# Kernel tuning notes

Hardware: AMD Instinct MI355X
Metric: run time of the kernel (lower is better)

The kernel has to match this reference:

```python
import jax, jax.numpy as jnp
import numpy as np

B, N, F, L = 16, 1536, 128, 2   # batch, input_features, enc(=dec)_features, n_layers
SLOPE = 0.2                      # LeakyReLU alpha
NEG = -1e9                       # mask fill for softmax


def setup_inputs() -> dict:
    key = jax.random.key(0)
    ks = jax.random.split(key, 14)
    g = lambda k, shape, s=0.05: (jax.random.normal(k, shape, jnp.float32) * s)
    data = jax.random.randint(ks[0], (B, N), 0, 2)          # binary presence vector
    embed = g(ks[1], (N + 1, F)).at[0].set(0.0)              # padding_idx=0 row zeroed
    return {
        "data": data,
        "embed": embed,
        "enc_W": g(ks[2], (L, F, F)),
        "enc_a_src": g(ks[3], (L, F)),
        "enc_a_dst": g(ks[4], (L, F)),
        "param_W": g(ks[5], (F, 2 * F)),
        "param_b": g(ks[6], (2 * F,)),
        "dec_W": g(ks[7], (F, F)),
        "dec_a_src": g(ks[8], (F,)),
        "dec_a_dst": g(ks[9], (F,)),
        "out_W1": g(ks[10], (F, F)),
        "out_b1": g(ks[11], (F,)),
        "out_W2": g(ks[12], (F, 1)),
        "out_b2": g(ks[13], (1,)),
    }


def _gat(x, mask, W, a_src, a_dst):
    """Single-head graph attention over a dense boolean adjacency `mask`.
    Equivalent to sparse GAT over the clique edge list data_to_edges() builds
    (self-loops included). Rows with no edges output 0."""
    h = x @ W                                    # (n, F)
    si = h @ a_src                               # (n,)
    sj = h @ a_dst                               # (n,)
    e = jax.nn.leaky_relu(si[:, None] + sj[None, :], SLOPE)
    e = jnp.where(mask, e, NEG)
    attn = jax.nn.softmax(e, axis=-1) * mask.any(axis=-1)[:, None]
    return attn @ h                              # (n, F)


def reference(data, embed, enc_W, enc_a_src, enc_a_dst, param_W, param_b,
              dec_W, dec_a_src, dec_a_dst, out_W1, out_b1, out_W2, out_b2):
    def per_sample(g):
        d = g != 0                               # active feature nodes
        m_in = d[:, None] & d[None, :]           # input clique adjacency (N, N)
        x = embed[:-1]                           # node features = embedding rows (N, F)
        for l in range(L):                       # encoder layers (n_layers=2)
            x = jax.nn.elu(_gat(x, m_in, enc_W[l], enc_a_src[l], enc_a_dst[l]))
        # variational parameterization (eval mode: dropout=id, reparam -> mean)
        par = x @ param_W + param_b              # (N, 2F)
        mean, sigma = par[:, :F], par[:, F:]
        w = (g == 1).astype(mean.dtype)
        cnt = jnp.maximum(w.sum(), 1.0)
        kld = 0.5 * jnp.sum(w[:, None] * (jnp.exp(sigma) - sigma - 1.0 + mean ** 2)) / cnt
        # append master node (last embedding row) and decode over extended clique
        enc_full = jnp.concatenate([mean, embed[-1:]], axis=0)      # (N+1, F)
        d_ext = jnp.concatenate([d, jnp.ones((1,), bool)])
        m_out = d_ext[:, None] & d_ext[None, :]                     # (N+1, N+1)
        dec = jax.nn.relu(_gat(enc_full, m_out, dec_W, dec_a_src, dec_a_dst))
        return dec[-1], kld                      # master-node readout (F,)

    feats, klds = jax.vmap(per_sample)(data)     # (B, F), (B,)
    pred = jax.nn.relu(feats @ out_W1 + out_b1) @ out_W2 + out_b2   # (B, 1)
    return pred, jnp.sum(klds)
```

## Files before the change

### kernel.cpp

```cpp
#include <hip/hip_runtime.h>

#define BB 16
#define NN 1536
#define FF 128
#define SLOPE 0.2f
#define NS 2048
#define CHS 64
#define NCH 24
#define TI 16
#define NPB (NN/8)
#define NDC 24

__global__ __launch_bounds__(1024) void k_sortpre(
    const int* __restrict__ data,
    const float* __restrict__ embed, const float* __restrict__ decW,
    const float* __restrict__ aS, const float* __restrict__ aD,
    const float* __restrict__ SJb, long sStride,
    int* __restrict__ actG, int* __restrict__ cntG,
    float* __restrict__ hN, float* __restrict__ sN,
    float* __restrict__ keyG, int* __restrict__ pjG,
    float* __restrict__ SBG, float* __restrict__ SDG)
{
  int b = blockIdx.x, t = threadIdx.x;
  if (b == BB){
    __shared__ float rs[2][2];
    if (t < FF){
      float acc = 0.f;
      for (int k=0;k<FF;++k) acc += embed[(long)NN*FF + k] * decW[k*FF + t];
      hN[t] = acc;
      float ps = acc * aS[t];
      float pd = acc * aD[t];
      #pragma unroll
      for (int o=32;o;o>>=1){ ps += __shfl_down(ps,o); pd += __shfl_down(pd,o); }
      if ((t&63)==0){ rs[0][t>>6]=ps; rs[1][t>>6]=pd; }
    }
    __syncthreads();
    if (t==0){ sN[0]=rs[0][0]+rs[0][1]; sN[1]=rs[1][0]+rs[1][1]; }
    return;
  }

  __shared__ float key[NS]; __shared__ int pj[NS];
  __shared__ float sb[NS]; __shared__ float sd[NS];
  __shared__ int cntS;
  int cnt;
  if (data != nullptr){
    __shared__ int s[256];
    const int PER = NN/256;
    int local[NN/256]; int nl = 0;
    if (t < 256){
      int base = t*PER;
      #pragma unroll
      for (int u=0; u<PER; ++u){
        if (data[b*NN + base + u] != 0) local[nl++] = base+u;
      }
      s[t]=nl;
    }
    __syncthreads();
    if (t==0){ int run=0; for (int i=0;i<256;i++){ int v=s[i]; s[i]=run; run+=v; }
               cntG[b]=run; cntS=run; }
    __syncthreads();
    if (t < 256){
      int o = s[t];
      for (int u=0; u<nl; ++u) actG[b*NN + o + u] = local[u];
    }
    __syncthreads();
    cnt = cntS;
  } else {
    cnt = cntG[b];
  }

  const float* SJ = SJb + (long)b*sStride;
  const int* act = (data != nullptr) ? actG + b*NN : nullptr;
  int NSort = 32; while (NSort < cnt) NSort <<= 1;

  for (int e=t; e<NSort; e+=1024){
    if (e<cnt){ int io = act ? act[e] : e; key[e]=SJ[io]; pj[e]=io; }
    else { key[e]=__builtin_inff(); pj[e]=0; }
  }
  __syncthreads();
  for (int k=2; k<=NSort; k<<=1){
    for (int j=k>>1; j>0; j>>=1){
      for (int e=t; e<NSort; e+=1024){
        int l = e ^ j;
        if (l > e){
          bool asc = ((e & k) == 0);
          float a0=key[e], a1=key[l];
          if (asc ? (a0>a1) : (a0<a1)){
            key[e]=a1; key[l]=a0; int p=pj[e]; pj[e]=pj[l]; pj[l]=p;
          }
        }
      }
      __syncthreads();
    }
  }
  for (int e=t; e<NSort; e+=1024){
    if (e<cnt){ float kk=key[e]; sb[e]=__expf(kk); sd[e]=__expf(SLOPE*kk); }
    else { sb[e]=0.f; sd[e]=0.f; }
  }
  __syncthreads();
  for (int off=1; off<NSort; off<<=1){
    float t0[2], t1[2]; int ne=0;
    for (int e=t; e<NSort; e+=1024){
      t0[ne] = (e>=off) ? sb[e-off] : 0.f;
      t1[ne] = (e>=off) ? sd[e-off] : 0.f;
      ne++;
    }
    __syncthreads();
    ne=0;
    for (int e=t; e<NSort; e+=1024){ sb[e]+=t0[ne]; sd[e]+=t1[ne]; ne++; }
    __syncthreads();
  }
  for (int e=t; e<cnt; e+=1024){
    keyG[(long)b*NN+e]=key[e]; pjG[(long)b*NN+e]=pj[e];
    SBG[(long)b*NN+e]=sb[e];   SDG[(long)b*NN+e]=sd[e];
  }
}

__global__ __launch_bounds__(128) void k_rowmm(const float* __restrict__ Xv,
    const float* __restrict__ W, const float* __restrict__ aS, const float* __restrict__ aD,
    float* __restrict__ H, float* __restrict__ SI, float* __restrict__ SJ)
{
  int r0 = blockIdx.x*8;
  int f = threadIdx.x;
  __shared__ float xs[8][FF];
  #pragma unroll
  for (int r=0;r<8;++r) xs[r][f] = Xv[(long)(r0+r)*FF + f];
  __syncthreads();
  float acc[8]={0.f,0.f,0.f,0.f,0.f,0.f,0.f,0.f};
  for (int k=0;k<FF;++k){
    float w = W[k*FF + f];
    #pragma unroll
    for (int r=0;r<8;++r) acc[r] += xs[r][k]*w;
  }
  float as = aS[f], ad = aD[f];
  __shared__ float red[2][8][2];
  #pragma unroll
  for (int r=0;r<8;++r){
    H[(long)(r0+r)*FF + f] = acc[r];
    float ps = acc[r]*as, pd = acc[r]*ad;
    #pragma unroll
    for (int o=32;o;o>>=1){ ps += __shfl_down(ps,o); pd += __shfl_down(pd,o); }
    if ((f&63)==0){ red[0][r][f>>6]=ps; red[1][r][f>>6]=pd; }
  }
  __syncthreads();
  if (f<8){
    SI[r0+f]=red[0][f][0]+red[0][f][1]; SJ[r0+f]=red[1][f][0]+red[1][f][1];
  }
}

__global__ __launch_bounds__(128) void k_chunk(
    const float* __restrict__ keyG, const int* __restrict__ pjG,
    const int* __restrict__ cntArr,
    const float* __restrict__ Hb, long hStride,
    float* __restrict__ PP, float* __restrict__ PM)
{
  int b = blockIdx.y, c = blockIdx.x, f = threadIdx.x;
  int cnt = cntArr[b];
  int k0 = c*CHS;
  if (k0 >= cnt) return;
  int k1 = k0+CHS; if (k1 > cnt) k1 = cnt;
  int kn = k1-k0;
  const float* H = Hb + (long)b*hStride + f;
  __shared__ int pjs[CHS]; __shared__ float wbs[CHS], wds[CHS];
  if (f < CHS && f < kn){
    float kk = keyG[(long)b*NN + k0 + f];
    pjs[f] = pjG[(long)b*NN + k0 + f];
    wbs[f] = __expf(kk);
    wds[f] = __expf(SLOPE*kk);
  }
  __syncthreads();
  float accB=0.f, accD=0.f;
  float hbuf[8];
  #pragma unroll
  for (int i=0;i<8;i++) hbuf[i] = (i<kn) ? H[(long)pjs[i]*FF] : 0.f;
  long obase = ((long)b*NN + k0)*FF + f;
  int k=0;
  for (; k+8<=kn; k+=8){
    #pragma unroll
    for (int u=0;u<8;u++){
      float hv = hbuf[u];
      int kp = k+u+8;
      hbuf[u] = (kp<kn) ? H[(long)pjs[kp]*FF] : 0.f;
      accB = fmaf(wbs[k+u], hv, accB);
      accD = fmaf(wds[k+u], hv, accD);
      PP[obase + (long)(k+u)*FF] = accB;
      PM[obase + (long)(k+u)*FF] = accD;
    }
  }
  for (; k<kn; ++k){
    float hv = H[(long)pjs[k]*FF];
    accB = fmaf(wbs[k], hv, accB);
    accD = fmaf(wds[k], hv, accD);
    PP[obase + (long)k*FF] = accB;
    PM[obase + (long)k*FF] = accD;
  }
}

__global__ __launch_bounds__(128) void k_aggout_mm(
    const float* __restrict__ keyG, const float* __restrict__ SBG, const float* __restrict__ SDG,
    const float* __restrict__ PP, const float* __restrict__ PM,
    const float* __restrict__ SI1, const int* __restrict__ actB,
    const int* __restrict__ cntArr,
    const float* __restrict__ W, const float* __restrict__ aS, const float* __restrict__ aD,
    float* __restrict__ Hout, float* __restrict__ SIo, float* __restrict__ SJo)
{
  int b = blockIdx.y;
  int cnt = cntArr[b];
  int r0 = blockIdx.x*TI;
  if (r0 >= cnt) return;
  int f = threadIdx.x;
  const int* act = actB + b*NN;
  __shared__ float keys[NN];
  __shared__ float offB[NCH][FF], offD[NCH][FF];
  __shared__ int kk[TI]; __shared__ float sis[TI];
  __shared__ float xs2[TI][FF];

  for (int e=f; e<cnt; e+=128) keys[e] = keyG[(long)b*NN + e];
  int nch = (cnt + CHS - 1)/CHS;
  for (int c=0; c<nch; ++c){
    int kend = (c+1)*CHS; if (kend > cnt) kend = cnt; kend -= 1;
    offB[c][f] = PP[((long)b*NN+kend)*FF+f];
    offD[c][f] = PM[((long)b*NN+kend)*FF+f];
  }
  float rb=0.f, rd=0.f;
  for (int c=0; c<nch; ++c){
    float tb=offB[c][f], td=offD[c][f];
    offB[c][f]=rb; offD[c][f]=rd;
    rb+=tb; rd+=td;
  }
  float TB = rb;
  __syncthreads();
  if (f < TI){
    int r = r0 + f;
    float si=0.f; int k=0;
    if (r < cnt){
      si = SI1[act[r]];
      float th = -si;
      int lo=0, hi=cnt;
      while (lo<hi){ int mid=(lo+hi)>>1; if (keys[mid]<=th) lo=mid+1; else hi=mid; }
      k = lo;
    }
    kk[f]=k; sis[f]=si;
  }
  __syncthreads();
  float TBs = SBG[(long)b*NN + (cnt-1)];
  int rmax = cnt - r0; if (rmax > TI) rmax = TI;
  for (int r=0; r<TI; ++r){
    float v = 0.f;
    if (r < rmax){
      int k = kk[r]; float si = sis[r];
      float PB=0.f, PD=0.f, SBv=0.f, SDv=0.f;
      if (k > 0){
        int c = (k-1)/CHS;
        PB = PP[((long)b*NN+(k-1))*FF+f] + offB[c][f];
        PD = PM[((long)b*NN+(k-1))*FF+f] + offD[c][f];
        SBv = SBG[(long)b*NN+(k-1)];
        SDv = SDG[(long)b*NN+(k-1)];
      }
      float ai=__expf(si), ci=__expf(SLOPE*si);
      float num = ai*(TB -PB ) + ci*PD;
      float den = ai*(TBs-SBv) + ci*SDv;
      float o2 = num/den;
      v = (o2>0.f)? o2 : (__expf(o2)-1.f);
    }
    xs2[r][f] = v;
  }
  __syncthreads();
  float acc2[TI];
  #pragma unroll
  for (int u=0;u<TI;++u) acc2[u]=0.f;
  for (int k=0;k<FF;++k){
    float w = W[k*FF + f];
    #pragma unroll
    for (int u=0;u<TI;++u) acc2[u] += xs2[u][k]*w;
  }
  float as = aS[f], ad = aD[f];
  __shared__ float red[2][TI][2];
  #pragma unroll
  for (int u=0;u<TI;++u){
    int rr=r0+u;
    if (rr<cnt) Hout[((long)b*NN+rr)*FF+f] = acc2[u];
    float ps = acc2[u]*as, pd = acc2[u]*ad;
    #pragma unroll
    for (int o=32;o;o>>=1){ ps += __shfl_down(ps,o); pd += __shfl_down(pd,o); }
    if ((f&63)==0){ red[0][u][f>>6]=ps; red[1][u][f>>6]=pd; }
  }
  __syncthreads();
  if (f < TI){
    int rr=r0+f;
    if (rr<cnt){
      SIo[(long)b*NN+rr]=red[0][f][0]+red[0][f][1];
      SJo[(long)b*NN+rr]=red[1][f][0]+red[1][f][1];
    }
  }
}

__global__ __launch_bounds__(128) void k_aggout(
    const float* __restrict__ keyG, const float* __restrict__ SBG, const float* __restrict__ SDG,
    const float* __restrict__ PP, const float* __restrict__ PM,
    const float* __restrict__ SIb,
    const int* __restrict__ cntArr, float* __restrict__ XoB)
{
  int b = blockIdx.y;
  int cnt = cntArr[b];
  int r0 = blockIdx.x*TI;
  if (r0 >= cnt) return;
  int f = threadIdx.x;
  const float* SI = SIb + (long)b*NN;
  float* xo = XoB + (long)b*NN*FF;
  __shared__ float keys[NN];
  __shared__ float offB[NCH][FF], offD[NCH][FF];
  __shared__ int kk[TI]; __shared__ float sis[TI];

  for (int e=f; e<cnt; e+=128) keys[e] = keyG[(long)b*NN + e];
  int nch = (cnt + CHS - 1)/CHS;
  for (int c=0; c<nch; ++c){
    int kend = (c+1)*CHS; if (kend > cnt) kend = cnt; kend -= 1;
    offB[c][f] = PP[((long)b*NN+kend)*FF+f];
    offD[c][f] = PM[((long)b*NN+kend)*FF+f];
  }
  float rb=0.f, rd=0.f;
  for (int c=0; c<nch; ++c){
    float tb=offB[c][f], td=offD[c][f];
    offB[c][f]=rb; offD[c][f]=rd;
    rb+=tb; rd+=td;
  }
  float TB = rb;
  __syncthreads();
  if (f < TI){
    int r = r0 + f;
    float si=0.f; int k=0;
    if (r < cnt){
      si = SI[r];
      float th = -si;
      int lo=0, hi=cnt;
      while (lo<hi){ int mid=(lo+hi)>>1; if (keys[mid]<=th) lo=mid+1; else hi=mid; }
      k = lo;
    }
    kk[f]=k; sis[f]=si;
  }
  __syncthreads();
  float TBs = SBG[(long)b*NN + (cnt-1)];
  int rmax = cnt - r0; if (rmax > TI) rmax = TI;
  for (int r=0; r<rmax; ++r){
    int k = kk[r]; float si = sis[r];
    float PB=0.f, PD=0.f, SBv=0.f, SDv=0.f;
    if (k > 0){
      int c = (k-1)/CHS;
      PB = PP[((long)b*NN+(k-1))*FF+f] + offB[c][f];
      PD = PM[((long)b*NN+(k-1))*FF+f] + offD[c][f];
      SBv = SBG[(long)b*NN+(k-1)];
      SDv = SDG[(long)b*NN+(k-1)];
    }
    float ai=__expf(si), ci=__expf(SLOPE*si);
    float num = ai*(TB -PB ) + ci*PD;
    float den = ai*(TBs-SBv) + ci*SDv;
    float o2 = num/den;
    xo[(long)(r0+r)*FF + f] = (o2>0.f)? o2 : (__expf(o2)-1.f);
  }
}

__global__ __launch_bounds__(256) void k_pardec(const float* __restrict__ XC,
    const float* __restrict__ pW, const float* __restrict__ pB,
    const float* __restrict__ decW, const float* __restrict__ dAd,
    float* __restrict__ KPART, float* __restrict__ H3, float* __restrict__ SJd,
    const int* __restrict__ cntArr)
{
  int b = blockIdx.y; int cnt = cntArr[b];
  int bx = blockIdx.x;
  int r0 = bx*8;
  int t = threadIdx.x;
  if (r0>=cnt){
    if (t==0) KPART[b*NPB + bx] = 0.f;
    return;
  }
  const float* X = XC + (long)b*NN*FF;
  __shared__ float xs[8][FF];
  for (int e=t; e<8*FF; e+=256){
    int r=e>>7, k=e&127; int rr=r0+r;
    xs[r][k] = (rr<cnt) ? X[(long)rr*FF+k] : 0.f;
  }
  __syncthreads();
  float acc[8]={0.f,0.f,0.f,0.f,0.f,0.f,0.f,0.f};
  for (int k=0;k<FF;++k){
    float w = pW[k*2*FF + t];
    #pragma unroll
    for (int r=0;r<8;++r) acc[r]+=xs[r][k]*w;
  }
  float bb = pB[t];
  float kacc=0.f;
  #pragma unroll
  for (int r=0;r<8;++r){
    int rr=r0+r;
    if (rr>=cnt) continue;
    float v = acc[r]+bb;
    if (t<FF) kacc += v*v;
    else kacc += __expf(v)-v-1.f;
  }
  #pragma unroll
  for (int o=32;o;o>>=1) kacc += __shfl_down(kacc,o);
  __shared__ float rw[4];
  if ((t&63)==0) rw[t>>6]=kacc;
  __syncthreads();
  if (t==0) KPART[b*NPB + bx] = rw[0]+rw[1]+rw[2]+rw[3];
  __shared__ float ms[8][FF];
  if (t < FF){
    #pragma unroll
    for (int r=0;r<8;++r){
      int rr=r0+r;
      ms[r][t] = (rr<cnt) ? acc[r]+bb : 0.f;
    }
  }
  __syncthreads();
  int h = t>>7, f = t&127;
  float a2[4]={0.f,0.f,0.f,0.f};
  for (int k=0;k<FF;++k){
    float w = decW[k*FF + f];
    #pragma unroll
    for (int u=0;u<4;++u) a2[u] += ms[h*4+u][k]*w;
  }
  float ad = dAd[f];
  __shared__ float redD[8][2];
  #pragma unroll
  for (int u=0;u<4;++u){
    int rq = h*4+u; int rr = r0+rq;
    if (rr<cnt) H3[((long)b*NN+rr)*FF+f] = a2[u];
    float pd = a2[u]*ad;
    #pragma unroll
    for (int o=32;o;o>>=1) pd += __shfl_down(pd,o);
    if ((t&63)==0) redD[rq][(t>>6)&1]=pd;
  }
  __syncthreads();
  if (t<8){
    int rr=r0+t;
    if (rr<cnt) SJd[(long)b*NN+rr]=redD[t][0]+redD[t][1];
  }
}

__global__ __launch_bounds__(128) void k_dec(const float* __restrict__ H3,
    const float* __restrict__ SJ3, const float* __restrict__ sN,
    const int* __restrict__ cntArr, float* __restrict__ DECP)
{
  int b=blockIdx.y, ch=blockIdx.x;
  int cnt=cntArr[b];
  int f=threadIdx.x;
  int r0=ch*CHS; int r1 = (r0+CHS < cnt) ? r0+CHS : cnt;
  float siN = sN[0];
  const float* H = H3 + (long)b*NN*FF;
  const float* SJ = SJ3 + (long)b*NN;
  float accV=0.f, accW=0.f;
  for (int r=r0;r<r1;++r){
    float sj=SJ[r]; float x=siN+sj;
    float e=(x>=0.f)? x : SLOPE*x;
    float w=__expf(e);
    accV += w*H[(long)r*FF+f];
    accW += w;
  }
  float* P = DECP + (long)(b*NDC+ch)*(FF+1);
  P[f]=accV;
  if (f==0) P[FF]=accW;
}

__global__ __launch_bounds__(128) void k_head(const float* __restrict__ DECP,
    const float* __restrict__ hN, const float* __restrict__ sN,
    const float* __restrict__ KPART, const int* __restrict__ cntArr,
    const float* __restrict__ W1, const float* __restrict__ b1,
    const float* __restrict__ W2, const float* __restrict__ b2,
    float* __restrict__ out)
{
  int b = blockIdx.x;
  int f = threadIdx.x;
  __shared__ float rw[2];
  if (b < BB){
    float siN=sN[0], sjN=sN[1];
    float xN=siN+sjN; float eN=(xN>=0.f)?xN:SLOPE*xN; float wN=__expf(eN);
    float num=0.f, den=0.f;
    for (int c=0;c<NDC;++c){
      const float* P = DECP + (long)(b*NDC+c)*(FF+1);
      num += P[f]; den += P[FF];
    }
    num += wN*hN[f]; den += wN;
    float v = num/den;
    __shared__ float feats[FF];
    feats[f] = (v>0.f)? v : 0.f;
    __syncthreads();
    float acc=0.f;
    for (int k=0;k<FF;++k) acc += feats[k]*W1[k*FF+f];
    acc += b1[f];
    acc = (acc>0.f)? acc : 0.f;
    float p = acc*W2[f];
    #pragma unroll
    for (int o=32;o;o>>=1) p += __shfl_down(p,o);
    if ((f&63)==0) rw[f>>6]=p;
    __syncthreads();
    if (f==0) out[b] = rw[0]+rw[1]+b2[0];
  } else {
    float s=0.f;
    for (int bb=0;bb<BB;++bb){
      float part=0.f;
      for (int c=f;c<NPB;c+=128) part += KPART[bb*NPB + c];
      #pragma unroll
      for (int o=32;o;o>>=1) part += __shfl_down(part,o);
      if ((f&63)==0) rw[f>>6]=part;
      __syncthreads();
      float tot = rw[0]+rw[1];
      int c=cntArr[bb]; float cf = (c>0)? (float)c : 1.f;
      s += 0.5f*tot/cf;
      __syncthreads();
    }
    if (f==0) out[16]=s;
  }
}

extern "C" void kernel_launch(void* const* d_in, const int* in_sizes, int n_in,
                              void* d_out, int out_size, void* d_ws, size_t ws_size,
                              hipStream_t stream)
{
  const int*   data  = (const int*)d_in[0];
  const float* embed = (const float*)d_in[1];
  const float* encW  = (const float*)d_in[2];
  const float* encAs = (const float*)d_in[3];
  const float* encAd = (const float*)d_in[4];
  const float* pW    = (const float*)d_in[5];
  const float* pB    = (const float*)d_in[6];
  const float* decW  = (const float*)d_in[7];
  const float* decAs = (const float*)d_in[8];
  const float* decAd = (const float*)d_in[9];
  const float* oW1   = (const float*)d_in[10];
  const float* oB1   = (const float*)d_in[11];
  const float* oW2   = (const float*)d_in[12];
  const float* oB2   = (const float*)d_in[13];
  float* out = (float*)d_out;

  float* w = (float*)d_ws;
  long o = 0;
  float* H1   = w+o; o += (long)NN*FF;
  float* H2   = w+o; o += (long)BB*NN*FF;
  float* XC   = w+o; o += (long)BB*NN*FF;
  float* PP   = w+o; o += (long)BB*NN*FF;
  float* PM   = w+o; o += (long)BB*NN*FF;
  float* SI1  = w+o; o += NN;
  float* SJ1  = w+o; o += NN;
  float* SI2  = w+o; o += (long)BB*NN;
  float* SJ2  = w+o; o += (long)BB*NN;
  float* KPART= w+o; o += (long)BB*NPB;
  float* hN   = w+o; o += FF;
  float* sN   = w+o; o += 2;
  float* DECP = w+o; o += (long)BB*NDC*(FF+1);
  float* keyG = w+o; o += (long)BB*NN;
  float* SBG  = w+o; o += (long)BB*NN;
  float* SDG  = w+o; o += (long)BB*NN;
  int* act = (int*)(w+o); o += (long)BB*NN;
  int* pjG = (int*)(w+o); o += (long)BB*NN;
  int* cnt = (int*)(w+o); o += BB;
  (void)in_sizes; (void)n_in; (void)out_size; (void)ws_size;

  k_rowmm<<<NN/8,128,0,stream>>>(embed, encW, encAs, encAd, H1, SI1, SJ1);
  k_sortpre<<<BB+1,1024,0,stream>>>(data, embed, decW, decAs, decAd,
      SJ1, 0L, act, cnt, hN, sN, keyG, pjG, SBG, SDG);
  k_chunk<<<dim3(NCH,BB),128,0,stream>>>(keyG, pjG, cnt, H1, 0L, PP, PM);
  k_aggout_mm<<<dim3(NN/TI,BB),128,0,stream>>>(keyG, SBG, SDG, PP, PM,
      SI1, act, cnt, encW + FF*FF, encAs + FF, encAd + FF, H2, SI2, SJ2);
  k_sortpre<<<BB,1024,0,stream>>>(nullptr, embed, decW, decAs, decAd,
      SJ2, (long)NN, act, cnt, hN, sN, keyG, pjG, SBG, SDG);
  k_chunk<<<dim3(NCH,BB),128,0,stream>>>(keyG, pjG, cnt, H2, (long)NN*FF, PP, PM);
  k_aggout<<<dim3(NN/TI,BB),128,0,stream>>>(keyG, SBG, SDG, PP, PM,
      SI2, cnt, XC);
  k_pardec<<<dim3(NPB,BB),256,0,stream>>>(XC, pW, pB, decW, decAd,
      KPART, H2 , SJ2 , cnt);
  k_dec<<<dim3(NDC,BB),128,0,stream>>>(H2 , SJ2, sN, cnt, DECP);
  k_head<<<BB+1,128,0,stream>>>(DECP, hN, sN, KPART, cnt, oW1, oB1, oW2, oB2, out);
}
```

Baseline: 276.1 us.

## Precompute chunk prefix offsets in separate kernel and shrink chunk and row tiles

Adds a k_offs kernel that computes the exclusive prefix sums of per-chunk totals once per batch. Previously every aggregation block recomputed these offsets into shared memory. Chunk size is halved to 32 so twice as many chunks run in parallel, and rows per aggregation block drop from 16 to 8, giving more blocks and less shared memory. The small matmul now reads four k values at a time from shared memory as float4. The cost is two extra kernel launches and global reads of the offset table.

```diff
diff --git a/kernel.cpp b/kernel.cpp
--- a/kernel.cpp
+++ b/kernel.cpp
@@ -5,10 +5,11 @@
 #define FF 128
 #define SLOPE 0.2f
 #define NS 2048
-#define CHS 64
-#define NCH 24
-#define TI 16
+#define CH2 32
+#define NCH2 48
+#define TI 8
 #define NPB (NN/8)
+#define DCS 64
 #define NDC 24
 
 __global__ __launch_bounds__(1024) void k_sortpre(
@@ -156,13 +157,13 @@
 {
   int b = blockIdx.y, c = blockIdx.x, f = threadIdx.x;
   int cnt = cntArr[b];
-  int k0 = c*CHS;
+  int k0 = c*CH2;
   if (k0 >= cnt) return;
-  int k1 = k0+CHS; if (k1 > cnt) k1 = cnt;
+  int k1 = k0+CH2; if (k1 > cnt) k1 = cnt;
   int kn = k1-k0;
   const float* H = Hb + (long)b*hStride + f;
-  __shared__ int pjs[CHS]; __shared__ float wbs[CHS], wds[CHS];
-  if (f < CHS && f < kn){
+  __shared__ int pjs[CH2]; __shared__ float wbs[CH2], wds[CH2];
+  if (f < CH2 && f < kn){
     float kk = keyG[(long)b*NN + k0 + f];
     pjs[f] = pjG[(long)b*NN + k0 + f];
     wbs[f] = __expf(kk);
@@ -196,9 +197,33 @@
   }
 }
 
+__global__ __launch_bounds__(128) void k_offs(
+    const float* __restrict__ PP, const float* __restrict__ PM,
+    const int* __restrict__ cntArr,
+    float* __restrict__ OFB, float* __restrict__ OFD)
+{
+  int b = blockIdx.x, f = threadIdx.x;
+  int cnt = cntArr[b];
+  float rb=0.f, rd=0.f;
+  long base = (long)b*(NCH2+1)*FF + f;
+  for (int c=0;c<NCH2;++c){
+    OFB[base + (long)c*FF] = rb;
+    OFD[base + (long)c*FF] = rd;
+    int k0 = c*CH2;
+    if (k0 < cnt){
+      int kend = k0+CH2; if (kend > cnt) kend = cnt; kend -= 1;
+      rb += PP[((long)b*NN+kend)*FF+f];
+      rd += PM[((long)b*NN+kend)*FF+f];
+    }
+  }
+  OFB[base + (long)NCH2*FF] = rb;
+  OFD[base + (long)NCH2*FF] = rd;
+}
+
 __global__ __launch_bounds__(128) void k_aggout_mm(
     const float* __restrict__ keyG, const float* __restrict__ SBG, const float* __restrict__ SDG,
     const float* __restrict__ PP, const float* __restrict__ PM,
+    const float* __restrict__ OFB, const float* __restrict__ OFD,
     const float* __restrict__ SI1, const int* __restrict__ actB,
     const int* __restrict__ cntArr,
     const float* __restrict__ W, const float* __restrict__ aS, const float* __restrict__ aD,
@@ -211,24 +236,10 @@
   int f = threadIdx.x;
   const int* act = actB + b*NN;
   __shared__ float keys[NN];
-  __shared__ float offB[NCH][FF], offD[NCH][FF];
   __shared__ int kk[TI]; __shared__ float sis[TI];
   __shared__ float xs2[TI][FF];
 
   for (int e=f; e<cnt; e+=128) keys[e] = keyG[(long)b*NN + e];
-  int nch = (cnt + CHS - 1)/CHS;
-  for (int c=0; c<nch; ++c){
-    int kend = (c+1)*CHS; if (kend > cnt) kend = cnt; kend -= 1;
-    offB[c][f] = PP[((long)b*NN+kend)*FF+f];
-    offD[c][f] = PM[((long)b*NN+kend)*FF+f];
-  }
-  float rb=0.f, rd=0.f;
-  for (int c=0; c<nch; ++c){
-    float tb=offB[c][f], td=offD[c][f];
-    offB[c][f]=rb; offD[c][f]=rd;
-    rb+=tb; rd+=td;
-  }
-  float TB = rb;
   __syncthreads();
   if (f < TI){
     int r = r0 + f;
@@ -243,6 +254,9 @@
     kk[f]=k; sis[f]=si;
   }
   __syncthreads();
+  const float* ofb = OFB + (long)b*(NCH2+1)*FF;
+  const float* ofd = OFD + (long)b*(NCH2+1)*FF;
+  float TB  = ofb[(long)NCH2*FF + f];
   float TBs = SBG[(long)b*NN + (cnt-1)];
   int rmax = cnt - r0; if (rmax > TI) rmax = TI;
   for (int r=0; r<TI; ++r){
@@ -251,9 +265,9 @@
       int k = kk[r]; float si = sis[r];
       float PB=0.f, PD=0.f, SBv=0.f, SDv=0.f;
       if (k > 0){
-        int c = (k-1)/CHS;
-        PB = PP[((long)b*NN+(k-1))*FF+f] + offB[c][f];
-        PD = PM[((long)b*NN+(k-1))*FF+f] + offD[c][f];
+        int c = (k-1)/CH2;
+        PB = PP[((long)b*NN+(k-1))*FF+f] + ofb[(long)c*FF+f];
+        PD = PM[((long)b*NN+(k-1))*FF+f] + ofd[(long)c*FF+f];
         SBv = SBG[(long)b*NN+(k-1)];
         SDv = SDG[(long)b*NN+(k-1)];
       }
@@ -269,10 +283,16 @@
   float acc2[TI];
   #pragma unroll
   for (int u=0;u<TI;++u) acc2[u]=0.f;
-  for (int k=0;k<FF;++k){
-    float w = W[k*FF + f];
-    #pragma unroll
-    for (int u=0;u<TI;++u) acc2[u] += xs2[u][k]*w;
+  for (int k=0;k<FF;k+=4){
+    float w0 = W[(k  )*FF + f];
+    float w1 = W[(k+1)*FF + f];
+    float w2 = W[(k+2)*FF + f];
+    float w3 = W[(k+3)*FF + f];
+    #pragma unroll
+    for (int u=0;u<TI;++u){
+      float4 x = *reinterpret_cast<const float4*>(&xs2[u][k]);
+      acc2[u] = fmaf(x.x,w0, fmaf(x.y,w1, fmaf(x.z,w2, fmaf(x.w,w3, acc2[u]))));
+    }
   }
   float as = aS[f], ad = aD[f];
   __shared__ float red[2][TI][2];
@@ -298,6 +318,7 @@
 __global__ __launch_bounds__(128) void k_aggout(
     const float* __restrict__ keyG, const float* __restrict__ SBG, const float* __restrict__ SDG,
     const float* __restrict__ PP, const float* __restrict__ PM,
+    const float* __restrict__ OFB, const float* __restrict__ OFD,
     const float* __restrict__ SIb,
     const int* __restrict__ cntArr, float* __restrict__ XoB)
 {
@@ -309,23 +330,9 @@
   const float* SI = SIb + (long)b*NN;
   float* xo = XoB + (long)b*NN*FF;
   __shared__ float keys[NN];
-  __shared__ float offB[NCH][FF], offD[NCH][FF];
   __shared__ int kk[TI]; __shared__ float sis[TI];
 
   for (int e=f; e<cnt; e+=128) keys[e] = keyG[(long)b*NN + e];
-  int nch = (cnt + CHS - 1)/CHS;
-  for (int c=0; c<nch; ++c){
-    int kend = (c+1)*CHS; if (kend > cnt) kend = cnt; kend -= 1;
-    offB[c][f] = PP[((long)b*NN+kend)*FF+f];
-    offD[c][f] = PM[((long)b*NN+kend)*FF+f];
-  }
-  float rb=0.f, rd=0.f;
-  for (int c=0; c<nch; ++c){
-    float tb=offB[c][f], td=offD[c][f];
-    offB[c][f]=rb; offD[c][f]=rd;
-    rb+=tb; rd+=td;
-  }
-  float TB = rb;
   __syncthreads();
   if (f < TI){
     int r = r0 + f;
@@ -340,15 +347,18 @@
     kk[f]=k; sis[f]=si;
   }
   __syncthreads();
+  const float* ofb = OFB + (long)b*(NCH2+1)*FF;
+  const float* ofd = OFD + (long)b*(NCH2+1)*FF;
+  float TB  = ofb[(long)NCH2*FF + f];
   float TBs = SBG[(long)b*NN + (cnt-1)];
   int rmax = cnt - r0; if (rmax > TI) rmax = TI;
   for (int r=0; r<rmax; ++r){
     int k = kk[r]; float si = sis[r];
     float PB=0.f, PD=0.f, SBv=0.f, SDv=0.f;
     if (k > 0){
-      int c = (k-1)/CHS;
-      PB = PP[((long)b*NN+(k-1))*FF+f] + offB[c][f];
-      PD = PM[((long)b*NN+(k-1))*FF+f] + offD[c][f];
+      int c = (k-1)/CH2;
+      PB = PP[((long)b*NN+(k-1))*FF+f] + ofb[(long)c*FF+f];
+      PD = PM[((long)b*NN+(k-1))*FF+f] + ofd[(long)c*FF+f];
       SBv = SBG[(long)b*NN+(k-1)];
       SDv = SDG[(long)b*NN+(k-1)];
     }
@@ -444,7 +454,7 @@
   int b=blockIdx.y, ch=blockIdx.x;
   int cnt=cntArr[b];
   int f=threadIdx.x;
-  int r0=ch*CHS; int r1 = (r0+CHS < cnt) ? r0+CHS : cnt;
+  int r0=ch*DCS; int r1 = (r0+DCS < cnt) ? r0+DCS : cnt;
   float siN = sN[0];
   const float* H = H3 + (long)b*NN*FF;
   const float* SJ = SJ3 + (long)b*NN;
@@ -550,6 +560,8 @@
   float* keyG = w+o; o += (long)BB*NN;
   float* SBG  = w+o; o += (long)BB*NN;
   float* SDG  = w+o; o += (long)BB*NN;
+  float* OFB  = w+o; o += (long)BB*(NCH2+1)*FF;
+  float* OFD  = w+o; o += (long)BB*(NCH2+1)*FF;
   int* act = (int*)(w+o); o += (long)BB*NN;
   int* pjG = (int*)(w+o); o += (long)BB*NN;
   int* cnt = (int*)(w+o); o += BB;
@@ -558,13 +570,15 @@
   k_rowmm<<<NN/8,128,0,stream>>>(embed, encW, encAs, encAd, H1, SI1, SJ1);
   k_sortpre<<<BB+1,1024,0,stream>>>(data, embed, decW, decAs, decAd,
       SJ1, 0L, act, cnt, hN, sN, keyG, pjG, SBG, SDG);
-  k_chunk<<<dim3(NCH,BB),128,0,stream>>>(keyG, pjG, cnt, H1, 0L, PP, PM);
-  k_aggout_mm<<<dim3(NN/TI,BB),128,0,stream>>>(keyG, SBG, SDG, PP, PM,
+  k_chunk<<<dim3(NCH2,BB),128,0,stream>>>(keyG, pjG, cnt, H1, 0L, PP, PM);
+  k_offs<<<BB,128,0,stream>>>(PP, PM, cnt, OFB, OFD);
+  k_aggout_mm<<<dim3(NN/TI,BB),128,0,stream>>>(keyG, SBG, SDG, PP, PM, OFB, OFD,
       SI1, act, cnt, encW + FF*FF, encAs + FF, encAd + FF, H2, SI2, SJ2);
   k_sortpre<<<BB,1024,0,stream>>>(nullptr, embed, decW, decAs, decAd,
       SJ2, (long)NN, act, cnt, hN, sN, keyG, pjG, SBG, SDG);
-  k_chunk<<<dim3(NCH,BB),128,0,stream>>>(keyG, pjG, cnt, H2, (long)NN*FF, PP, PM);
-  k_aggout<<<dim3(NN/TI,BB),128,0,stream>>>(keyG, SBG, SDG, PP, PM,
+  k_chunk<<<dim3(NCH2,BB),128,0,stream>>>(keyG, pjG, cnt, H2, (long)NN*FF, PP, PM);
+  k_offs<<<BB,128,0,stream>>>(PP, PM, cnt, OFB, OFD);
+  k_aggout<<<dim3(NN/TI,BB),128,0,stream>>>(keyG, SBG, SDG, PP, PM, OFB, OFD,
       SI2, cnt, XC);
   k_pardec<<<dim3(NPB,BB),256,0,stream>>>(XC, pW, pB, decW, decAd,
       KPART, H2 , SJ2 , cnt);
```

Result: no change. 278.2 us (+0.8%).
